# Kernel optimization log

Measured on AMD Instinct MI355X. Metric: run time of the kernel, lower is better.

The kernel has to match this reference:

```python
import jax, jax.numpy as jnp
import numpy as np

N = 50000
E = 800000
IN, HID, OUT = 256, 128, 64
BN_EPS = 1e-5

def sage(x, src, dst, Wl, bl, Wr):
    # PyG SAGEConv (aggr='mean'): lin_l(mean_j x_j) + lin_r(x_root)
    agg = jax.ops.segment_sum(x[src], dst, num_segments=N)
    deg = jax.ops.segment_sum(jnp.ones((src.shape[0], 1), x.dtype), dst, num_segments=N)
    mean_agg = agg / jnp.maximum(deg, 1.0)
    return mean_agg @ Wl + bl + x @ Wr

def bn_eval(x, gamma, beta):
    # eval-mode BatchNorm1d with running_mean=0, running_var=1
    return x * (gamma / jnp.sqrt(1.0 + BN_EPS)) + beta

def setup_inputs() -> dict:
    key = jax.random.key(0)
    ks = jax.random.split(key, 16)
    g = lambda k, shp, s: jax.random.normal(k, shp, jnp.float32) * s
    inp = {
        'x': g(ks[0], (N, IN), 1.0),
        'edge_index': jax.random.randint(ks[1], (2, E), 0, N, jnp.int32),
        'eps': g(ks[2], (10, N, OUT), 1.0),
        'W1l': g(ks[3], (IN, HID), 0.06), 'b1': jnp.zeros((HID,), jnp.float32), 'W1r': g(ks[4], (IN, HID), 0.06),
        'g1': jnp.ones((HID,), jnp.float32), 'be1': jnp.zeros((HID,), jnp.float32),
        'W2l': g(ks[5], (HID, 2 * HID), 0.09), 'b2': jnp.zeros((2 * HID,), jnp.float32), 'W2r': g(ks[6], (HID, 2 * HID), 0.09),
        'g2': jnp.ones((2 * HID,), jnp.float32), 'be2': jnp.zeros((2 * HID,), jnp.float32),
        'W3l': g(ks[7], (2 * HID, 2 * OUT), 0.06), 'b3': jnp.zeros((2 * OUT,), jnp.float32), 'W3r': g(ks[8], (2 * HID, 2 * OUT), 0.06),
        'Wd1': g(ks[9], (OUT, HID), 0.12), 'bd1': jnp.zeros((HID,), jnp.float32),
        'g3': jnp.ones((HID,), jnp.float32), 'be3': jnp.zeros((HID,), jnp.float32),
        'Wd2': g(ks[10], (HID, IN), 0.09), 'bd2': jnp.zeros((IN,), jnp.float32),
    }
    return inp

def reference(x, edge_index, eps, W1l, b1, W1r, g1, be1, W2l, b2, W2r, g2, be2,
              W3l, b3, W3r, Wd1, bd1, g3, be3, Wd2, bd2):
    src, dst = edge_index[0], edge_index[1]
    # encode (dropout is identity in eval mode)
    x1 = bn_eval(jax.nn.relu(sage(x, src, dst, W1l, b1, W1r)), g1, be1)
    x2 = bn_eval(jax.nn.relu(sage(x1, src, dst, W2l, b2, W2r)), g2, be2)
    mz = sage(x2, src, dst, W3l, b3, W3r)
    mean, log_std = mz[:, :OUT], mz[:, OUT:]
    # reparameterize: average of n_samples draws == mean + std * mean(eps)
    std = jnp.exp(log_std)
    z = mean + std * jnp.mean(eps, axis=0)
    # decode
    h = bn_eval(jax.nn.relu(z @ Wd1 + bd1), g3, be3) + x1
    return h @ Wd2 + bd2
```

## Files before the change

kernel.cpp:

```cpp
#include <hip/hip_runtime.h>


typedef unsigned short u16;
typedef short bf16x8 __attribute__((ext_vector_type(8)));
typedef float f32x4  __attribute__((ext_vector_type(4)));

constexpr float BN_EPS = 1e-5f;

__device__ __forceinline__ u16 f2bf(float f) {
    unsigned u = __float_as_uint(f);
    return (u16)((u + 0x7FFFu + ((u >> 16) & 1u)) >> 16);
}
__device__ __forceinline__ float bf2f(u16 h) {
    return __uint_as_float(((unsigned)h) << 16);
}
__device__ __forceinline__ void gl_lds16(const void* g, void* l) {
    __builtin_amdgcn_global_load_lds(
        (const __attribute__((address_space(1))) unsigned*)g,
        (__attribute__((address_space(3))) unsigned*)l, 16, 0, 0);
}

template<int KS>
__device__ __forceinline__ void stage_panel(const u16* g, char* lb, int k0, int t) {
    const int sr   = t >> 2;
    const int sq   = (t & 3) ^ ((t >> 3) & 3);
    const int wave = t >> 6;
    gl_lds16(g + (size_t)sr * KS + k0 + sq * 8,        lb + wave * 1024);
    gl_lds16(g + (size_t)(sr + 64) * KS + k0 + sq * 8, lb + 4096 + wave * 1024);
}


__global__ void hist_kernel(const int* __restrict__ dst, int E, int* __restrict__ deg) {
    int e = blockIdx.x * 256 + threadIdx.x;
    if (e < E) atomicAdd(&deg[dst[e]], 1);
}

__global__ __launch_bounds__(256)
void scan_partial(const int* __restrict__ deg, int N, int* __restrict__ bsum) {
    __shared__ int sd[256];
    int i = blockIdx.x * 256 + threadIdx.x;
    int v = (i < N) ? deg[i] : 0;
    sd[threadIdx.x] = v;
    __syncthreads();
    for (int off = 128; off > 0; off >>= 1) {
        if (threadIdx.x < off) sd[threadIdx.x] += sd[threadIdx.x + off];
        __syncthreads();
    }
    if (threadIdx.x == 0) bsum[blockIdx.x] = sd[0];
}

__global__ __launch_bounds__(256)
void scan_final2(const int* __restrict__ deg, const int* __restrict__ bsum,
                 int N, int E, int* __restrict__ row_ptr, int* __restrict__ cursor,
                 float* __restrict__ inv_deg) {
    __shared__ int sd[256];
    int t = threadIdx.x;
    int partial = 0;
    for (int j = t; j < blockIdx.x; j += 256) partial += bsum[j];
    sd[t] = partial;
    __syncthreads();
    for (int off = 128; off > 0; off >>= 1) {
        if (t < off) sd[t] += sd[t + off];
        __syncthreads();
    }
    int base = sd[0];
    __syncthreads();
    int i = blockIdx.x * 256 + t;
    int d = (i < N) ? deg[i] : 0;
    sd[t] = d;
    __syncthreads();
    for (int off = 1; off < 256; off <<= 1) {
        int u = (t >= off) ? sd[t - off] : 0;
        __syncthreads();
        sd[t] += u;
        __syncthreads();
    }
    if (i < N) {
        int excl = base + sd[t] - d;
        row_ptr[i] = excl;
        cursor[i]  = excl;
        inv_deg[i] = 1.0f / (float)max(d, 1);
        if (i == N - 1) row_ptr[N] = E;
    }
}

__global__ void fill_kernel(const int* __restrict__ src, const int* __restrict__ dst,
                            int E, int* __restrict__ cursor, int* __restrict__ csr) {
    int e = blockIdx.x * 256 + threadIdx.x;
    if (e < E) {
        int p = atomicAdd(&cursor[dst[e]], 1);
        csr[p] = src[e];
    }
}


__global__ void pack_cast(const float* __restrict__ x,
                          const float* __restrict__ W1l, const float* __restrict__ W1r,
                          const float* __restrict__ W2l, const float* __restrict__ W2r,
                          const float* __restrict__ W3l, const float* __restrict__ W3r,
                          const float* __restrict__ Wd1, const float* __restrict__ Wd2,
                          u16* __restrict__ Bt1, u16* __restrict__ Bt2,
                          u16* __restrict__ Bt3, u16* __restrict__ Btd1,
                          u16* __restrict__ Btd2, u16* __restrict__ xb,
                          int N, int Mpad) {
    int idx = blockIdx.x * 256 + threadIdx.x;
    if (idx < 65536) {
        int c = idx >> 8, k = idx & 255;
        float v = (c < 128) ? W1l[k * 128 + c] : W1r[k * 128 + (c - 128)];
        Bt1[c * 256 + k] = f2bf(v);
    } else if (idx < 131072) {
        int i2 = idx - 65536;
        int c = i2 >> 8, k = i2 & 255;
        float v = (k < 128) ? W2l[k * 256 + c] : W2r[(k - 128) * 256 + c];
        Bt2[c * 256 + k] = f2bf(v);
    } else if (idx < 196608) {
        int i2 = idx - 131072;
        int c = i2 >> 8, k = i2 & 255;
        float v = (c < 128) ? W3l[k * 128 + c] : W3r[k * 128 + (c - 128)];
        Bt3[c * 256 + k] = f2bf(v);
    } else if (idx < 204800) {
        int i2 = idx - 196608;
        int c = i2 >> 6, k = i2 & 63;
        Btd1[i2] = f2bf(Wd1[k * 128 + c]);
    } else if (idx < 237568) {
        int i2 = idx - 204800;
        int c = i2 >> 7, k = i2 & 127;
        Btd2[i2] = f2bf(Wd2[k * 256 + c]);
    }
    if (idx < Mpad * 64) {
        int row = idx >> 6, q = idx & 63;
        float4 v = make_float4(0.f, 0.f, 0.f, 0.f);
        if (row < N) v = *(const float4*)&x[(size_t)row * 256 + q * 4];
        ushort4 o;
        o.x = f2bf(v.x); o.y = f2bf(v.y); o.z = f2bf(v.z); o.w = f2bf(v.w);
        *(ushort4*)&xb[(size_t)row * 256 + q * 4] = o;
    }
}


template<int K, int NC, int EPI, bool F32OUT>
__global__ __launch_bounds__(256)
void mgemm(const u16* __restrict__ A, const u16* __restrict__ Bt,
           const float* __restrict__ bias, const float* __restrict__ gamma,
           const float* __restrict__ beta,
           const u16* __restrict__ skip, int skip_ld,
           void* __restrict__ Cout, int M) {
    __shared__ char lds[32768];
    char* As0 = lds;
    char* As1 = lds + 8192;
    char* Bs0 = lds + 16384;
    char* Bs1 = lds + 24576;

    const int t = threadIdx.x;
    const int l = t & 63;
    const int wave = t >> 6;
    const int wr = wave >> 1, wc = wave & 1;
    const int lr = l & 15, kg = l >> 4;
    const int row0 = blockIdx.x * 128;
    const int col0 = blockIdx.y * 128;

    f32x4 acc[4][4];
    #pragma unroll
    for (int m = 0; m < 4; m++)
        #pragma unroll
        for (int n = 0; n < 4; n++)
            #pragma unroll
            for (int r = 0; r < 4; r++) acc[m][n][r] = 0.f;

    const u16* Ab = A  + (size_t)row0 * K;
    const u16* Bb = Bt + (size_t)col0 * K;

    stage_panel<K>(Ab, As0, 0, t);
    stage_panel<K>(Bb, Bs0, 0, t);
    __syncthreads();

    const int swz = (kg ^ ((lr >> 1) & 3)) << 4;
    constexpr int NT = K / 32;
    for (int ks = 0; ks < NT; ks++) {
        char* Ac = (ks & 1) ? As1 : As0;
        char* Bc = (ks & 1) ? Bs1 : Bs0;
        if (ks + 1 < NT) {
            stage_panel<K>(Ab, (ks & 1) ? As0 : As1, (ks + 1) * 32, t);
            stage_panel<K>(Bb, (ks & 1) ? Bs0 : Bs1, (ks + 1) * 32, t);
        }
        bf16x8 af[4], bfr[4];
        #pragma unroll
        for (int m = 0; m < 4; m++)
            af[m] = *(const bf16x8*)(Ac + wr * 4096 + m * 1024 + lr * 64 + swz);
        #pragma unroll
        for (int n = 0; n < 4; n++)
            bfr[n] = *(const bf16x8*)(Bc + wc * 4096 + n * 1024 + lr * 64 + swz);
        #pragma unroll
        for (int m = 0; m < 4; m++)
            #pragma unroll
            for (int n = 0; n < 4; n++)
                acc[m][n] = __builtin_amdgcn_mfma_f32_16x16x32_bf16(
                    af[m], bfr[n], acc[m][n], 0, 0, 0);
        __syncthreads();
    }

    const float rs = rsqrtf(1.0f + BN_EPS);
    const int colb = col0 + wc * 64;
    const int rowb = row0 + wr * 64;
    float bia[4], gpr[4], bet[4];
    if (EPI == 1 || EPI == 2) {
        #pragma unroll
        for (int n = 0; n < 4; n++) {
            int c = colb + n * 16 + lr;
            bia[n] = bias[c];
            gpr[n] = gamma[c] * rs;
            bet[n] = beta[c];
        }
    } else if (EPI == 3) {
        #pragma unroll
        for (int n = 0; n < 4; n++) bia[n] = bias[colb + n * 16 + lr];
    }
    __syncthreads();

    char* rp = lds + wave * 4096;
    #pragma unroll
    for (int m = 0; m < 4; m++) {
        #pragma unroll
        for (int n = 0; n < 4; n++) {
            #pragma unroll
            for (int r = 0; r < 4; r++) {
                float v = acc[m][n][r];
                if (EPI == 1 || EPI == 2) {
                    v += bia[n];
                    v = fmaxf(v, 0.f);
                    v = v * gpr[n] + bet[n];
                }
                if (EPI == 2)
                    v += bf2f(skip[(size_t)(rowb + m * 16 + kg * 4 + r) * skip_ld
                                   + colb + n * 16 + lr]);
                if (EPI == 3) v += bia[n];
                int rl = kg * 4 + r, cl = n * 16 + lr;
                if (F32OUT) ((float*)rp)[rl * 64 + cl] = v;
                else        ((u16*)rp)[rl * 64 + cl]   = f2bf(v);
            }
        }
        if (F32OUT) {
            float* rpf = (float*)rp;
            #pragma unroll
            for (int rr = 0; rr < 4; rr++) {
                int rloc = rr * 4 + kg;
                int grow = rowb + m * 16 + rloc;
                if (grow < M) {
                    f32x4 v4 = *(f32x4*)&rpf[rloc * 64 + lr * 4];
                    *(f32x4*)((float*)Cout + (size_t)grow * NC + colb + lr * 4) = v4;
                }
            }
        } else {
            u16* rph = (u16*)rp;
            #pragma unroll
            for (int hh = 0; hh < 2; hh++) {
                int rloc = hh * 8 + (l >> 3);
                int grow = rowb + m * 16 + rloc;
                bf16x8 v8 = *(bf16x8*)&rph[rloc * 64 + (l & 7) * 8];
                *(bf16x8*)((u16*)Cout + (size_t)grow * NC + colb + (l & 7) * 8) = v8;
            }
        }
    }
}


__global__ __launch_bounds__(256)
void dec_fused(const u16* __restrict__ zb, const u16* __restrict__ Btd1,
               const u16* __restrict__ Btd2, const float* __restrict__ bd1,
               const float* __restrict__ g3, const float* __restrict__ be3,
               const u16* __restrict__ x1, const float* __restrict__ bd2,
               float* __restrict__ out, int M) {
    __shared__ char lds[65536];
    const int t = threadIdx.x;
    const int l = t & 63;
    const int wave = t >> 6;
    const int wr = wave >> 1, wc = wave & 1;
    const int lr = l & 15, kg = l >> 4;
    const int row0 = blockIdx.x * 128;
    const float rs = rsqrtf(1.0f + BN_EPS);
    const int swz = (kg ^ ((lr >> 1) & 3)) << 4;
    char* hb = lds + 32768;

    stage_panel<64>(zb + (size_t)row0 * 64, lds,         0, t);
    stage_panel<64>(zb + (size_t)row0 * 64, lds + 8192, 32, t);
    stage_panel<64>(Btd1, lds + 16384,  0, t);
    stage_panel<64>(Btd1, lds + 24576, 32, t);
    __syncthreads();

    f32x4 acc[4][4];
    #pragma unroll
    for (int m = 0; m < 4; m++)
        #pragma unroll
        for (int n = 0; n < 4; n++)
            #pragma unroll
            for (int r = 0; r < 4; r++) acc[m][n][r] = 0.f;

    #pragma unroll
    for (int ks = 0; ks < 2; ks++) {
        char* Ac = lds + ks * 8192;
        char* Bc = lds + 16384 + ks * 8192;
        bf16x8 af[4], bfr[4];
        #pragma unroll
        for (int m = 0; m < 4; m++)
            af[m] = *(const bf16x8*)(Ac + wr * 4096 + m * 1024 + lr * 64 + swz);
        #pragma unroll
        for (int n = 0; n < 4; n++)
            bfr[n] = *(const bf16x8*)(Bc + wc * 4096 + n * 1024 + lr * 64 + swz);
        #pragma unroll
        for (int m = 0; m < 4; m++)
            #pragma unroll
            for (int n = 0; n < 4; n++)
                acc[m][n] = __builtin_amdgcn_mfma_f32_16x16x32_bf16(
                    af[m], bfr[n], acc[m][n], 0, 0, 0);
    }

    {
        float bia[4], gpr[4], bet[4];
        #pragma unroll
        for (int n = 0; n < 4; n++) {
            int c = wc * 64 + n * 16 + lr;
            bia[n] = bd1[c];
            gpr[n] = g3[c] * rs;
            bet[n] = be3[c];
        }
        #pragma unroll
        for (int m = 0; m < 4; m++)
            #pragma unroll
            for (int n = 0; n < 4; n++)
                #pragma unroll
                for (int r = 0; r < 4; r++) {
                    int rl = wr * 64 + m * 16 + kg * 4 + r;
                    int cl = wc * 64 + n * 16 + lr;
                    float v = acc[m][n][r] + bia[n];
                    v = fmaxf(v, 0.f) * gpr[n] + bet[n];
                    v += bf2f(x1[(size_t)(row0 + rl) * 256 + cl]);
                    int slot = (cl >> 3) ^ (rl & 7);
                    ((u16*)(hb + rl * 256 + slot * 16))[cl & 7] = f2bf(v);
                }
    }
    __syncthreads();

    for (int ch = 0; ch < 2; ch++) {
        const u16* Bb2 = Btd2 + ch * 16384;
        stage_panel<128>(Bb2, lds, 0, t);
        #pragma unroll
        for (int m = 0; m < 4; m++)
            #pragma unroll
            for (int n = 0; n < 4; n++)
                #pragma unroll
                for (int r = 0; r < 4; r++) acc[m][n][r] = 0.f;
        __syncthreads();

        for (int ks = 0; ks < 4; ks++) {
            char* Bc = lds + (ks & 1) * 8192;
            if (ks + 1 < 4)
                stage_panel<128>(Bb2, lds + (((ks & 1) ^ 1) * 8192), (ks + 1) * 32, t);
            bf16x8 af[4], bfr[4];
            #pragma unroll
            for (int m = 0; m < 4; m++) {
                int row = wr * 64 + m * 16 + lr;
                int s = (ks * 4 + kg) ^ (row & 7);
                af[m] = *(const bf16x8*)(hb + row * 256 + s * 16);
            }
            #pragma unroll
            for (int n = 0; n < 4; n++)
                bfr[n] = *(const bf16x8*)(Bc + wc * 4096 + n * 1024 + lr * 64 + swz);
            #pragma unroll
            for (int m = 0; m < 4; m++)
                #pragma unroll
                for (int n = 0; n < 4; n++)
                    acc[m][n] = __builtin_amdgcn_mfma_f32_16x16x32_bf16(
                        af[m], bfr[n], acc[m][n], 0, 0, 0);
            __syncthreads();
        }

        const int colb = ch * 128 + wc * 64;
        const int rowb = row0 + wr * 64;
        float b2v[4];
        #pragma unroll
        for (int n = 0; n < 4; n++) b2v[n] = bd2[colb + n * 16 + lr];
        char* rp = lds + wave * 4096;
        #pragma unroll
        for (int m = 0; m < 4; m++) {
            #pragma unroll
            for (int n = 0; n < 4; n++)
                #pragma unroll
                for (int r = 0; r < 4; r++)
                    ((float*)rp)[(kg * 4 + r) * 64 + n * 16 + lr] = acc[m][n][r] + b2v[n];
            float* rpf = (float*)rp;
            #pragma unroll
            for (int rr = 0; rr < 4; rr++) {
                int rloc = rr * 4 + kg;
                int grow = rowb + m * 16 + rloc;
                if (grow < M) {
                    f32x4 v4 = *(f32x4*)&rpf[rloc * 64 + lr * 4];
                    *(f32x4*)&out[(size_t)grow * 256 + colb + lr * 4] = v4;
                }
            }
        }
        __syncthreads();
    }
}


__global__ __launch_bounds__(256)
void agg1_kernel(const u16* __restrict__ Y1, const int* __restrict__ row_ptr,
                 const int* __restrict__ csr, const float* __restrict__ inv_deg,
                 const float* __restrict__ b1, const float* __restrict__ g1,
                 const float* __restrict__ be1, u16* __restrict__ catX, int N) {
    int g   = (blockIdx.x * 256 + threadIdx.x) >> 4;
    int sub = threadIdx.x & 15;
    if (g >= N) return;
    int b = row_ptr[g], e = row_ptr[g + 1];
    const int off = sub * 8;
    float a[8] = {};
    int ee = b;
    for (; ee + 3 < e; ee += 4) {
        int j0 = csr[ee], j1 = csr[ee + 1], j2 = csr[ee + 2], j3 = csr[ee + 3];
        bf16x8 v0 = *(const bf16x8*)&Y1[(size_t)j0 * 256 + off];
        bf16x8 v1 = *(const bf16x8*)&Y1[(size_t)j1 * 256 + off];
        bf16x8 v2 = *(const bf16x8*)&Y1[(size_t)j2 * 256 + off];
        bf16x8 v3 = *(const bf16x8*)&Y1[(size_t)j3 * 256 + off];
        #pragma unroll
        for (int r = 0; r < 8; r++)
            a[r] += (bf2f((u16)v0[r]) + bf2f((u16)v1[r]))
                  + (bf2f((u16)v2[r]) + bf2f((u16)v3[r]));
    }
    for (; ee < e; ee++) {
        bf16x8 v0 = *(const bf16x8*)&Y1[(size_t)csr[ee] * 256 + off];
        #pragma unroll
        for (int r = 0; r < 8; r++) a[r] += bf2f((u16)v0[r]);
    }
    float id = inv_deg[g];
    bf16x8 u = *(const bf16x8*)&Y1[(size_t)g * 256 + 128 + off];
    const float rs = rsqrtf(1.0f + BN_EPS);
    bf16x8 o;
    #pragma unroll
    for (int r = 0; r < 8; r++) {
        int c = off + r;
        float v = a[r] * id + b1[c] + bf2f((u16)u[r]);
        v = fmaxf(v, 0.f);
        v = v * (g1[c] * rs) + be1[c];
        o[r] = (short)f2bf(v);
    }
    *(bf16x8*)&catX[(size_t)g * 256 + 128 + off] = o;
}

__global__ __launch_bounds__(256)
void agg2_kernel(const int* __restrict__ row_ptr, const int* __restrict__ csr,
                 const float* __restrict__ inv_deg, u16* __restrict__ catX, int N) {
    int g   = (blockIdx.x * 256 + threadIdx.x) >> 4;
    int sub = threadIdx.x & 15;
    if (g >= N) return;
    int b = row_ptr[g], e = row_ptr[g + 1];
    const int off = sub * 8;
    float a[8] = {};
    int ee = b;
    for (; ee + 3 < e; ee += 4) {
        int j0 = csr[ee], j1 = csr[ee + 1], j2 = csr[ee + 2], j3 = csr[ee + 3];
        bf16x8 v0 = *(const bf16x8*)&catX[(size_t)j0 * 256 + 128 + off];
        bf16x8 v1 = *(const bf16x8*)&catX[(size_t)j1 * 256 + 128 + off];
        bf16x8 v2 = *(const bf16x8*)&catX[(size_t)j2 * 256 + 128 + off];
        bf16x8 v3 = *(const bf16x8*)&catX[(size_t)j3 * 256 + 128 + off];
        #pragma unroll
        for (int r = 0; r < 8; r++)
            a[r] += (bf2f((u16)v0[r]) + bf2f((u16)v1[r]))
                  + (bf2f((u16)v2[r]) + bf2f((u16)v3[r]));
    }
    for (; ee < e; ee++) {
        bf16x8 v0 = *(const bf16x8*)&catX[(size_t)csr[ee] * 256 + 128 + off];
        #pragma unroll
        for (int r = 0; r < 8; r++) a[r] += bf2f((u16)v0[r]);
    }
    float id = inv_deg[g];
    bf16x8 o;
    #pragma unroll
    for (int r = 0; r < 8; r++) o[r] = (short)f2bf(a[r] * id);
    *(bf16x8*)&catX[(size_t)g * 256 + off] = o;
}

__global__ __launch_bounds__(256)
void agg3_kernel(const u16* __restrict__ Y3, const int* __restrict__ row_ptr,
                 const int* __restrict__ csr, const float* __restrict__ inv_deg,
                 const float* __restrict__ b3, const float* __restrict__ eps,
                 u16* __restrict__ z, int N) {
    int g   = (blockIdx.x * 256 + threadIdx.x) >> 4;
    int sub = threadIdx.x & 15;
    if (g >= N) return;
    int b = row_ptr[g], e = row_ptr[g + 1];
    const int off = sub * 8;

    f32x4 emv = {0.f, 0.f, 0.f, 0.f};
    #pragma unroll
    for (int t10 = 0; t10 < 10; t10++) {
        f32x4 v = *(const f32x4*)&eps[((size_t)t10 * N + g) * 64 + sub * 4];
        emv += v;
    }
    emv *= 0.1f;

    float a[8] = {};
    int ee = b;
    for (; ee + 3 < e; ee += 4) {
        int j0 = csr[ee], j1 = csr[ee + 1], j2 = csr[ee + 2], j3 = csr[ee + 3];
        bf16x8 v0 = *(const bf16x8*)&Y3[(size_t)j0 * 256 + off];
        bf16x8 v1 = *(const bf16x8*)&Y3[(size_t)j1 * 256 + off];
        bf16x8 v2 = *(const bf16x8*)&Y3[(size_t)j2 * 256 + off];
        bf16x8 v3 = *(const bf16x8*)&Y3[(size_t)j3 * 256 + off];
        #pragma unroll
        for (int r = 0; r < 8; r++)
            a[r] += (bf2f((u16)v0[r]) + bf2f((u16)v1[r]))
                  + (bf2f((u16)v2[r]) + bf2f((u16)v3[r]));
    }
    for (; ee < e; ee++) {
        bf16x8 v0 = *(const bf16x8*)&Y3[(size_t)csr[ee] * 256 + off];
        #pragma unroll
        for (int r = 0; r < 8; r++) a[r] += bf2f((u16)v0[r]);
    }
    float id = inv_deg[g];
    bf16x8 u = *(const bf16x8*)&Y3[(size_t)g * 256 + 128 + off];
    float mzv[8];
    #pragma unroll
    for (int r = 0; r < 8; r++)
        mzv[r] = a[r] * id + b3[off + r] + bf2f((u16)u[r]);

    const int wl = threadIdx.x & 63;
    const int wb = wl & ~15;
    const int s0 = wb + ((2 * sub) & 15);
    const int s1 = wb + ((2 * sub + 1) & 15);
    float em8[8];
    #pragma unroll
    for (int q = 0; q < 4; q++) {
        em8[q]     = __shfl(emv[q], s0);
        em8[4 + q] = __shfl(emv[q], s1);
    }
    float hi[8];
    #pragma unroll
    for (int r = 0; r < 8; r++) hi[r] = __shfl_xor(mzv[r], 8);

    if (sub < 8) {
        bf16x8 o;
        #pragma unroll
        for (int r = 0; r < 8; r++)
            o[r] = (short)f2bf(mzv[r] + expf(hi[r]) * em8[r]);
        *(bf16x8*)&z[(size_t)g * 64 + sub * 8] = o;
    }
}


extern "C" void kernel_launch(void* const* d_in, const int* in_sizes, int n_in,
                              void* d_out, int out_size, void* d_ws, size_t ws_size,
                              hipStream_t stream) {
    const float* x    = (const float*)d_in[0];
    const int*   ei   = (const int*)d_in[1];
    const float* eps  = (const float*)d_in[2];
    const float* W1l  = (const float*)d_in[3];
    const float* b1   = (const float*)d_in[4];
    const float* W1r  = (const float*)d_in[5];
    const float* g1   = (const float*)d_in[6];
    const float* be1  = (const float*)d_in[7];
    const float* W2l  = (const float*)d_in[8];
    const float* b2   = (const float*)d_in[9];
    const float* W2r  = (const float*)d_in[10];
    const float* g2   = (const float*)d_in[11];
    const float* be2  = (const float*)d_in[12];
    const float* W3l  = (const float*)d_in[13];
    const float* b3   = (const float*)d_in[14];
    const float* W3r  = (const float*)d_in[15];
    const float* Wd1  = (const float*)d_in[16];
    const float* bd1  = (const float*)d_in[17];
    const float* g3   = (const float*)d_in[18];
    const float* be3  = (const float*)d_in[19];
    const float* Wd2  = (const float*)d_in[20];
    const float* bd2  = (const float*)d_in[21];

    const int Nn   = in_sizes[0] / 256;
    const int E    = in_sizes[1] / 2;
    const int Mpad = ((Nn + 127) / 128) * 128;
    const int* srcp = ei;
    const int* dstp = ei + E;
    const int nb = (Nn + 255) / 256;

    char* w = (char*)d_ws;
    auto alloc = [&](size_t bytes) -> void* {
        void* p = (void*)w;
        w += (bytes + 255) & ~(size_t)255;
        return p;
    };
    int*   deg     = (int*)  alloc((size_t)Nn * 4);
    int*   bsum    = (int*)  alloc((size_t)nb * 4);
    int*   row_ptr = (int*)  alloc((size_t)(Nn + 1) * 4);
    int*   cursor  = (int*)  alloc((size_t)Nn * 4);
    float* inv_deg = (float*)alloc((size_t)Nn * 4);
    int*   csr     = (int*)  alloc((size_t)E * 4);
    u16*   Bt1     = (u16*)  alloc(256 * 256 * 2);
    u16*   Bt2     = (u16*)  alloc(256 * 256 * 2);
    u16*   Bt3     = (u16*)  alloc(256 * 256 * 2);
    u16*   Btd1    = (u16*)  alloc(128 * 64 * 2);
    u16*   Btd2    = (u16*)  alloc(256 * 128 * 2);
    u16*   xb      = (u16*)  alloc((size_t)Mpad * 256 * 2);
    u16*   zb      = (u16*)  alloc((size_t)Mpad * 64 * 2);
    u16*   bufA    = (u16*)  alloc((size_t)Mpad * 256 * 2);
    u16*   bufB    = (u16*)  alloc((size_t)Mpad * 256 * 2);
    u16*   bufC    = (u16*)  alloc((size_t)Mpad * 256 * 2);
    if ((size_t)(w - (char*)d_ws) > ws_size) return;

    hipMemsetAsync(deg, 0, (size_t)Nn * 4, stream);
    hist_kernel<<<(E + 255) / 256, 256, 0, stream>>>(dstp, E, deg);
    scan_partial<<<nb, 256, 0, stream>>>(deg, Nn, bsum);
    scan_final2<<<nb, 256, 0, stream>>>(deg, bsum, Nn, E, row_ptr, cursor, inv_deg);
    fill_kernel<<<(E + 255) / 256, 256, 0, stream>>>(srcp, dstp, E, cursor, csr);

    pack_cast<<<(Mpad * 64 + 255) / 256, 256, 0, stream>>>(
        x, W1l, W1r, W2l, W2r, W3l, W3r, Wd1, Wd2,
        Bt1, Bt2, Bt3, Btd1, Btd2, xb, Nn, Mpad);

    dim3 g2c(Mpad / 128, 2);
    const int aggBlocks = (Nn + 15) / 16;

    mgemm<256, 256, 0, false><<<g2c, 256, 0, stream>>>(
        xb, Bt1, nullptr, nullptr, nullptr, nullptr, 0, bufA, Mpad);
    agg1_kernel<<<aggBlocks, 256, 0, stream>>>(bufA, row_ptr, csr, inv_deg,
                                               b1, g1, be1, bufB, Nn);
    agg2_kernel<<<aggBlocks, 256, 0, stream>>>(row_ptr, csr, inv_deg, bufB, Nn);
    mgemm<256, 256, 1, false><<<g2c, 256, 0, stream>>>(
        bufB, Bt2, b2, g2, be2, nullptr, 0, bufA, Mpad);
    mgemm<256, 256, 0, false><<<g2c, 256, 0, stream>>>(
        bufA, Bt3, nullptr, nullptr, nullptr, nullptr, 0, bufC, Mpad);
    agg3_kernel<<<aggBlocks, 256, 0, stream>>>(bufC, row_ptr, csr, inv_deg,
                                               b3, eps, zb, Nn);
    dec_fused<<<Mpad / 128, 256, 0, stream>>>(
        zb, Btd1, Btd2, bd1, g3, be3, bufB + 128, bd2, (float*)d_out, Nn);
}
```

Measured before the change: 302.7 us.

## Fuse histogram into pack, degree-sort aggregation rows, fuse layer2/3 GEMMs

Merges the edge histogram into the weight/feature pack kernel to save a launch. Adds a degree-bucketed permutation so the aggregation kernels process nodes grouped by similar degree, which reduces divergence and load imbalance within a block. Fuses the layer-2 and layer-3 GEMMs into one kernel that keeps the intermediate activation in LDS, avoiding a global round trip. The fused GEMM uses 72KB of LDS, which may lower occupancy, and the permutation scatters output writes.

```diff
diff --git a/kernel.cpp b/kernel.cpp
--- a/kernel.cpp
+++ b/kernel.cpp
@@ -30,80 +30,18 @@
 }
 
 
-__global__ void hist_kernel(const int* __restrict__ dst, int E, int* __restrict__ deg) {
-    int e = blockIdx.x * 256 + threadIdx.x;
-    if (e < E) atomicAdd(&deg[dst[e]], 1);
-}
-
-__global__ __launch_bounds__(256)
-void scan_partial(const int* __restrict__ deg, int N, int* __restrict__ bsum) {
-    __shared__ int sd[256];
-    int i = blockIdx.x * 256 + threadIdx.x;
-    int v = (i < N) ? deg[i] : 0;
-    sd[threadIdx.x] = v;
-    __syncthreads();
-    for (int off = 128; off > 0; off >>= 1) {
-        if (threadIdx.x < off) sd[threadIdx.x] += sd[threadIdx.x + off];
-        __syncthreads();
-    }
-    if (threadIdx.x == 0) bsum[blockIdx.x] = sd[0];
-}
-
-__global__ __launch_bounds__(256)
-void scan_final2(const int* __restrict__ deg, const int* __restrict__ bsum,
-                 int N, int E, int* __restrict__ row_ptr, int* __restrict__ cursor,
-                 float* __restrict__ inv_deg) {
-    __shared__ int sd[256];
-    int t = threadIdx.x;
-    int partial = 0;
-    for (int j = t; j < blockIdx.x; j += 256) partial += bsum[j];
-    sd[t] = partial;
-    __syncthreads();
-    for (int off = 128; off > 0; off >>= 1) {
-        if (t < off) sd[t] += sd[t + off];
-        __syncthreads();
-    }
-    int base = sd[0];
-    __syncthreads();
-    int i = blockIdx.x * 256 + t;
-    int d = (i < N) ? deg[i] : 0;
-    sd[t] = d;
-    __syncthreads();
-    for (int off = 1; off < 256; off <<= 1) {
-        int u = (t >= off) ? sd[t - off] : 0;
-        __syncthreads();
-        sd[t] += u;
-        __syncthreads();
-    }
-    if (i < N) {
-        int excl = base + sd[t] - d;
-        row_ptr[i] = excl;
-        cursor[i]  = excl;
-        inv_deg[i] = 1.0f / (float)max(d, 1);
-        if (i == N - 1) row_ptr[N] = E;
-    }
-}
-
-__global__ void fill_kernel(const int* __restrict__ src, const int* __restrict__ dst,
-                            int E, int* __restrict__ cursor, int* __restrict__ csr) {
-    int e = blockIdx.x * 256 + threadIdx.x;
-    if (e < E) {
-        int p = atomicAdd(&cursor[dst[e]], 1);
-        csr[p] = src[e];
-    }
-}
-
-
-__global__ void pack_cast(const float* __restrict__ x,
-                          const float* __restrict__ W1l, const float* __restrict__ W1r,
-                          const float* __restrict__ W2l, const float* __restrict__ W2r,
-                          const float* __restrict__ W3l, const float* __restrict__ W3r,
-                          const float* __restrict__ Wd1, const float* __restrict__ Wd2,
-                          u16* __restrict__ Bt1, u16* __restrict__ Bt2,
-                          u16* __restrict__ Bt3, u16* __restrict__ Btd1,
-                          u16* __restrict__ Btd2, u16* __restrict__ xb,
-                          int N, int Mpad) {
+__global__ void histpack(const int* __restrict__ dst, int E, int* __restrict__ deg,
+                         const float* __restrict__ x,
+                         const float* __restrict__ W1l, const float* __restrict__ W1r,
+                         const float* __restrict__ W2l, const float* __restrict__ W2r,
+                         const float* __restrict__ W3l, const float* __restrict__ W3r,
+                         const float* __restrict__ Wd1, const float* __restrict__ Wd2,
+                         u16* __restrict__ Bt1, u16* __restrict__ Bt2,
+                         u16* __restrict__ Bt3, u16* __restrict__ Btd1,
+                         u16* __restrict__ Btd2, u16* __restrict__ xb,
+                         int N, int Mpad) {
     int idx = blockIdx.x * 256 + threadIdx.x;
+    if (idx < E) atomicAdd(&deg[dst[idx]], 1);
     if (idx < 65536) {
         int c = idx >> 8, k = idx & 255;
         float v = (c < 128) ? W1l[k * 128 + c] : W1r[k * 128 + (c - 128)];
@@ -137,13 +75,94 @@
     }
 }
 
-
-template<int K, int NC, int EPI, bool F32OUT>
+__global__ __launch_bounds__(256)
+void scan_partial(const int* __restrict__ deg, int N, int* __restrict__ bsum,
+                  int* __restrict__ bins) {
+    __shared__ int sd[256];
+    __shared__ int lbins[64];
+    int i = blockIdx.x * 256 + threadIdx.x;
+    int v = (i < N) ? deg[i] : 0;
+    sd[threadIdx.x] = v;
+    if (threadIdx.x < 64) lbins[threadIdx.x] = 0;
+    __syncthreads();
+    if (i < N) atomicAdd(&lbins[min(v, 63)], 1);
+    for (int off = 128; off > 0; off >>= 1) {
+        if (threadIdx.x < off) sd[threadIdx.x] += sd[threadIdx.x + off];
+        __syncthreads();
+    }
+    if (threadIdx.x == 0) bsum[blockIdx.x] = sd[0];
+    if (threadIdx.x < 64) {
+        int c = lbins[threadIdx.x];
+        if (c) atomicAdd(&bins[threadIdx.x], c);
+    }
+}
+
+__global__ void bin_scan(const int* __restrict__ bins, int* __restrict__ bincur) {
+    __shared__ int sd[64];
+    int t = threadIdx.x;
+    int v = bins[t];
+    sd[t] = v;
+    __syncthreads();
+    for (int off = 1; off < 64; off <<= 1) {
+        int u = (t >= off) ? sd[t - off] : 0;
+        __syncthreads();
+        sd[t] += u;
+        __syncthreads();
+    }
+    bincur[t] = sd[t] - v;
+}
+
+__global__ __launch_bounds__(256)
+void scan_final2(const int* __restrict__ deg, const int* __restrict__ bsum,
+                 int N, int E, int* __restrict__ row_ptr, int* __restrict__ cursor,
+                 float* __restrict__ inv_deg, int* __restrict__ bincur,
+                 int* __restrict__ perm) {
+    __shared__ int sd[256];
+    int t = threadIdx.x;
+    int partial = 0;
+    for (int j = t; j < blockIdx.x; j += 256) partial += bsum[j];
+    sd[t] = partial;
+    __syncthreads();
+    for (int off = 128; off > 0; off >>= 1) {
+        if (t < off) sd[t] += sd[t + off];
+        __syncthreads();
+    }
+    int base = sd[0];
+    __syncthreads();
+    int i = blockIdx.x * 256 + t;
+    int d = (i < N) ? deg[i] : 0;
+    sd[t] = d;
+    __syncthreads();
+    for (int off = 1; off < 256; off <<= 1) {
+        int u = (t >= off) ? sd[t - off] : 0;
+        __syncthreads();
+        sd[t] += u;
+        __syncthreads();
+    }
+    if (i < N) {
+        int excl = base + sd[t] - d;
+        row_ptr[i] = excl;
+        cursor[i]  = excl;
+        inv_deg[i] = 1.0f / (float)max(d, 1);
+        if (i == N - 1) row_ptr[N] = E;
+        int pos = atomicAdd(&bincur[min(d, 63)], 1);
+        perm[pos] = i;
+    }
+}
+
+__global__ void fill_kernel(const int* __restrict__ src, const int* __restrict__ dst,
+                            int E, int* __restrict__ cursor, int* __restrict__ csr) {
+    int e = blockIdx.x * 256 + threadIdx.x;
+    if (e < E) {
+        int p = atomicAdd(&cursor[dst[e]], 1);
+        csr[p] = src[e];
+    }
+}
+
+
+template<int K, int NC>
 __global__ __launch_bounds__(256)
 void mgemm(const u16* __restrict__ A, const u16* __restrict__ Bt,
-           const float* __restrict__ bias, const float* __restrict__ gamma,
-           const float* __restrict__ beta,
-           const u16* __restrict__ skip, int skip_ld,
            void* __restrict__ Cout, int M) {
     __shared__ char lds[32768];
     char* As0 = lds;
@@ -199,66 +218,176 @@
         __syncthreads();
     }
 
-    const float rs = rsqrtf(1.0f + BN_EPS);
     const int colb = col0 + wc * 64;
     const int rowb = row0 + wr * 64;
-    float bia[4], gpr[4], bet[4];
-    if (EPI == 1 || EPI == 2) {
+    __syncthreads();
+
+    char* rp = lds + wave * 4096;
+    #pragma unroll
+    for (int m = 0; m < 4; m++) {
+        #pragma unroll
+        for (int n = 0; n < 4; n++)
+            #pragma unroll
+            for (int r = 0; r < 4; r++) {
+                int rl = kg * 4 + r, cl = n * 16 + lr;
+                ((u16*)rp)[rl * 64 + cl] = f2bf(acc[m][n][r]);
+            }
+        u16* rph = (u16*)rp;
+        #pragma unroll
+        for (int hh = 0; hh < 2; hh++) {
+            int rloc = hh * 8 + (l >> 3);
+            int grow = rowb + m * 16 + rloc;
+            bf16x8 v8 = *(bf16x8*)&rph[rloc * 64 + (l & 7) * 8];
+            if (grow < M)
+                *(bf16x8*)((u16*)Cout + (size_t)grow * NC + colb + (l & 7) * 8) = v8;
+        }
+    }
+}
+
+
+__global__ __launch_bounds__(256)
+void gemm23(const u16* __restrict__ catX, const u16* __restrict__ Bt2,
+            const u16* __restrict__ Bt3,
+            const float* __restrict__ b2, const float* __restrict__ g2,
+            const float* __restrict__ be2,
+            u16* __restrict__ Y3, int M) {
+    __shared__ char lds[73728];
+    char* Ad0 = lds;
+    char* Ad1 = lds + 4096;
+    char* Bd0 = lds + 8192;
+    char* Bd1 = lds + 8192 + 16384;
+    char* hb  = lds + 40960;
+
+    const int t = threadIdx.x;
+    const int l = t & 63;
+    const int wave = t >> 6;
+    const int lr = l & 15, kg = l >> 4;
+    const int row0 = blockIdx.x * 64;
+    const int swz = (kg ^ ((lr >> 1) & 3)) << 4;
+    const int sr = t >> 2;
+    const int sq = (t & 3) ^ ((t >> 3) & 3);
+    const float rs = rsqrtf(1.0f + BN_EPS);
+
+    const u16* Ab = catX + (size_t)row0 * 256;
+
+    auto stageA = [&](char* buf, int k0) {
+        gl_lds16(Ab + (size_t)sr * 256 + k0 + sq * 8, buf + wave * 1024);
+    };
+    auto stageB = [&](const u16* Bt, char* buf, int k0) {
+        #pragma unroll
+        for (int q = 0; q < 4; q++)
+            gl_lds16(Bt + (size_t)(q * 64 + sr) * 256 + k0 + sq * 8,
+                     buf + q * 4096 + wave * 1024);
+    };
+
+    f32x4 acc[4][4];
+    #pragma unroll
+    for (int m = 0; m < 4; m++)
+        #pragma unroll
+        for (int n = 0; n < 4; n++)
+            #pragma unroll
+            for (int r = 0; r < 4; r++) acc[m][n][r] = 0.f;
+
+    stageA(Ad0, 0);
+    stageB(Bt2, Bd0, 0);
+    __syncthreads();
+    for (int ks = 0; ks < 8; ks++) {
+        char* Ac = (ks & 1) ? Ad1 : Ad0;
+        char* Bc = (ks & 1) ? Bd1 : Bd0;
+        if (ks < 7) {
+            stageA((ks & 1) ? Ad0 : Ad1, (ks + 1) * 32);
+            stageB(Bt2, (ks & 1) ? Bd0 : Bd1, (ks + 1) * 32);
+        }
+        bf16x8 af[4], bfr[4];
+        #pragma unroll
+        for (int m = 0; m < 4; m++)
+            af[m] = *(const bf16x8*)(Ac + m * 1024 + lr * 64 + swz);
+        #pragma unroll
+        for (int n = 0; n < 4; n++)
+            bfr[n] = *(const bf16x8*)(Bc + wave * 4096 + n * 1024 + lr * 64 + swz);
+        #pragma unroll
+        for (int m = 0; m < 4; m++)
+            #pragma unroll
+            for (int n = 0; n < 4; n++)
+                acc[m][n] = __builtin_amdgcn_mfma_f32_16x16x32_bf16(
+                    af[m], bfr[n], acc[m][n], 0, 0, 0);
+        __syncthreads();
+    }
+
+    stageB(Bt3, Bd0, 0);
+
+    {
+        float bia[4], gpr[4], bet[4];
         #pragma unroll
         for (int n = 0; n < 4; n++) {
-            int c = colb + n * 16 + lr;
-            bia[n] = bias[c];
-            gpr[n] = gamma[c] * rs;
-            bet[n] = beta[c];
-        }
-    } else if (EPI == 3) {
-        #pragma unroll
-        for (int n = 0; n < 4; n++) bia[n] = bias[colb + n * 16 + lr];
-    }
-    __syncthreads();
+            int c = wave * 64 + n * 16 + lr;
+            bia[n] = b2[c];
+            gpr[n] = g2[c] * rs;
+            bet[n] = be2[c];
+        }
+        #pragma unroll
+        for (int m = 0; m < 4; m++)
+            #pragma unroll
+            for (int n = 0; n < 4; n++)
+                #pragma unroll
+                for (int r = 0; r < 4; r++) {
+                    int rl = m * 16 + kg * 4 + r;
+                    int cl = wave * 64 + n * 16 + lr;
+                    float v = acc[m][n][r] + bia[n];
+                    v = fmaxf(v, 0.f) * gpr[n] + bet[n];
+                    int slot = (cl >> 3) ^ (rl & 7);
+                    ((u16*)(hb + rl * 512 + slot * 16))[cl & 7] = f2bf(v);
+                }
+    }
+    __syncthreads();
+
+    #pragma unroll
+    for (int m = 0; m < 4; m++)
+        #pragma unroll
+        for (int n = 0; n < 4; n++)
+            #pragma unroll
+            for (int r = 0; r < 4; r++) acc[m][n][r] = 0.f;
+
+    for (int ks = 0; ks < 8; ks++) {
+        char* Bc = (ks & 1) ? Bd1 : Bd0;
+        if (ks < 7) stageB(Bt3, (ks & 1) ? Bd0 : Bd1, (ks + 1) * 32);
+        bf16x8 af[4], bfr[4];
+        #pragma unroll
+        for (int m = 0; m < 4; m++) {
+            int row = m * 16 + lr;
+            int s = (ks * 4 + kg) ^ (row & 7);
+            af[m] = *(const bf16x8*)(hb + row * 512 + s * 16);
+        }
+        #pragma unroll
+        for (int n = 0; n < 4; n++)
+            bfr[n] = *(const bf16x8*)(Bc + wave * 4096 + n * 1024 + lr * 64 + swz);
+        #pragma unroll
+        for (int m = 0; m < 4; m++)
+            #pragma unroll
+            for (int n = 0; n < 4; n++)
+                acc[m][n] = __builtin_amdgcn_mfma_f32_16x16x32_bf16(
+                    af[m], bfr[n], acc[m][n], 0, 0, 0);
+        __syncthreads();
+    }
 
     char* rp = lds + wave * 4096;
     #pragma unroll
     for (int m = 0; m < 4; m++) {
         #pragma unroll
-        for (int n = 0; n < 4; n++) {
+        for (int n = 0; n < 4; n++)
             #pragma unroll
             for (int r = 0; r < 4; r++) {
-                float v = acc[m][n][r];
-                if (EPI == 1 || EPI == 2) {
-                    v += bia[n];
-                    v = fmaxf(v, 0.f);
-                    v = v * gpr[n] + bet[n];
-                }
-                if (EPI == 2)
-                    v += bf2f(skip[(size_t)(rowb + m * 16 + kg * 4 + r) * skip_ld
-                                   + colb + n * 16 + lr]);
-                if (EPI == 3) v += bia[n];
                 int rl = kg * 4 + r, cl = n * 16 + lr;
-                if (F32OUT) ((float*)rp)[rl * 64 + cl] = v;
-                else        ((u16*)rp)[rl * 64 + cl]   = f2bf(v);
+                ((u16*)rp)[rl * 64 + cl] = f2bf(acc[m][n][r]);
             }
-        }
-        if (F32OUT) {
-            float* rpf = (float*)rp;
-            #pragma unroll
-            for (int rr = 0; rr < 4; rr++) {
-                int rloc = rr * 4 + kg;
-                int grow = rowb + m * 16 + rloc;
-                if (grow < M) {
-                    f32x4 v4 = *(f32x4*)&rpf[rloc * 64 + lr * 4];
-                    *(f32x4*)((float*)Cout + (size_t)grow * NC + colb + lr * 4) = v4;
-                }
-            }
-        } else {
-            u16* rph = (u16*)rp;
-            #pragma unroll
-            for (int hh = 0; hh < 2; hh++) {
-                int rloc = hh * 8 + (l >> 3);
-                int grow = rowb + m * 16 + rloc;
-                bf16x8 v8 = *(bf16x8*)&rph[rloc * 64 + (l & 7) * 8];
-                *(bf16x8*)((u16*)Cout + (size_t)grow * NC + colb + (l & 7) * 8) = v8;
-            }
+        u16* rph = (u16*)rp;
+        #pragma unroll
+        for (int hh = 0; hh < 2; hh++) {
+            int rloc = hh * 8 + (l >> 3);
+            int grow = row0 + m * 16 + rloc;
+            bf16x8 v8 = *(bf16x8*)&rph[rloc * 64 + (l & 7) * 8];
+            if (grow < M)
+                *(bf16x8*)&Y3[(size_t)grow * 256 + wave * 64 + (l & 7) * 8] = v8;
         }
     }
 }
@@ -406,11 +535,13 @@
 __global__ __launch_bounds__(256)
 void agg1_kernel(const u16* __restrict__ Y1, const int* __restrict__ row_ptr,
                  const int* __restrict__ csr, const float* __restrict__ inv_deg,
+                 const int* __restrict__ perm,
                  const float* __restrict__ b1, const float* __restrict__ g1,
                  const float* __restrict__ be1, u16* __restrict__ catX, int N) {
-    int g   = (blockIdx.x * 256 + threadIdx.x) >> 4;
+    int gid = (blockIdx.x * 256 + threadIdx.x) >> 4;
     int sub = threadIdx.x & 15;
-    if (g >= N) return;
+    if (gid >= N) return;
+    int g = perm[gid];
     int b = row_ptr[g], e = row_ptr[g + 1];
     const int off = sub * 8;
     float a[8] = {};
@@ -448,10 +579,12 @@
 
 __global__ __launch_bounds__(256)
 void agg2_kernel(const int* __restrict__ row_ptr, const int* __restrict__ csr,
-                 const float* __restrict__ inv_deg, u16* __restrict__ catX, int N) {
-    int g   = (blockIdx.x * 256 + threadIdx.x) >> 4;
+                 const float* __restrict__ inv_deg, const int* __restrict__ perm,
+                 u16* __restrict__ catX, int N) {
+    int gid = (blockIdx.x * 256 + threadIdx.x) >> 4;
     int sub = threadIdx.x & 15;
-    if (g >= N) return;
+    if (gid >= N) return;
+    int g = perm[gid];
     int b = row_ptr[g], e = row_ptr[g + 1];
     const int off = sub * 8;
     float a[8] = {};
@@ -482,11 +615,13 @@
 __global__ __launch_bounds__(256)
 void agg3_kernel(const u16* __restrict__ Y3, const int* __restrict__ row_ptr,
                  const int* __restrict__ csr, const float* __restrict__ inv_deg,
+                 const int* __restrict__ perm,
                  const float* __restrict__ b3, const float* __restrict__ eps,
                  u16* __restrict__ z, int N) {
-    int g   = (blockIdx.x * 256 + threadIdx.x) >> 4;
+    int gid = (blockIdx.x * 256 + threadIdx.x) >> 4;
     int sub = threadIdx.x & 15;
-    if (g >= N) return;
+    if (gid >= N) return;
+    int g = perm[gid];
     int b = row_ptr[g], e = row_ptr[g + 1];
     const int off = sub * 8;
 
@@ -587,6 +722,9 @@
         return p;
     };
     int*   deg     = (int*)  alloc((size_t)Nn * 4);
+    int*   bins    = (int*)  alloc(64 * 4);
+    int*   bincur  = (int*)  alloc(64 * 4);
+    int*   perm    = (int*)  alloc((size_t)Nn * 4);
     int*   bsum    = (int*)  alloc((size_t)nb * 4);
     int*   row_ptr = (int*)  alloc((size_t)(Nn + 1) * 4);
     int*   cursor  = (int*)  alloc((size_t)Nn * 4);
@@ -604,29 +742,27 @@
     u16*   bufC    = (u16*)  alloc((size_t)Mpad * 256 * 2);
     if ((size_t)(w - (char*)d_ws) > ws_size) return;
 
-    hipMemsetAsync(deg, 0, (size_t)Nn * 4, stream);
-    hist_kernel<<<(E + 255) / 256, 256, 0, stream>>>(dstp, E, deg);
-    scan_partial<<<nb, 256, 0, stream>>>(deg, Nn, bsum);
-    scan_final2<<<nb, 256, 0, stream>>>(deg, bsum, Nn, E, row_ptr, cursor, inv_deg);
+    size_t degpad = ((size_t)Nn * 4 + 255) & ~(size_t)255;
+    hipMemsetAsync(deg, 0, degpad + 256, stream);
+
+    histpack<<<(Mpad * 64 + 255) / 256, 256, 0, stream>>>(
+        dstp, E, deg, x, W1l, W1r, W2l, W2r, W3l, W3r, Wd1, Wd2,
+        Bt1, Bt2, Bt3, Btd1, Btd2, xb, Nn, Mpad);
+    scan_partial<<<nb, 256, 0, stream>>>(deg, Nn, bsum, bins);
+    bin_scan<<<1, 64, 0, stream>>>(bins, bincur);
+    scan_final2<<<nb, 256, 0, stream>>>(deg, bsum, Nn, E, row_ptr, cursor,
+                                        inv_deg, bincur, perm);
     fill_kernel<<<(E + 255) / 256, 256, 0, stream>>>(srcp, dstp, E, cursor, csr);
-
-    pack_cast<<<(Mpad * 64 + 255) / 256, 256, 0, stream>>>(
-        x, W1l, W1r, W2l, W2r, W3l, W3r, Wd1, Wd2,
-        Bt1, Bt2, Bt3, Btd1, Btd2, xb, Nn, Mpad);
 
     dim3 g2c(Mpad / 128, 2);
     const int aggBlocks = (Nn + 15) / 16;
 
-    mgemm<256, 256, 0, false><<<g2c, 256, 0, stream>>>(
-        xb, Bt1, nullptr, nullptr, nullptr, nullptr, 0, bufA, Mpad);
-    agg1_kernel<<<aggBlocks, 256, 0, stream>>>(bufA, row_ptr, csr, inv_deg,
+    mgemm<256, 256><<<g2c, 256, 0, stream>>>(xb, Bt1, bufA, Mpad);
+    agg1_kernel<<<aggBlocks, 256, 0, stream>>>(bufA, row_ptr, csr, inv_deg, perm,
                                                b1, g1, be1, bufB, Nn);
-    agg2_kernel<<<aggBlocks, 256, 0, stream>>>(row_ptr, csr, inv_deg, bufB, Nn);
-    mgemm<256, 256, 1, false><<<g2c, 256, 0, stream>>>(
-        bufB, Bt2, b2, g2, be2, nullptr, 0, bufA, Mpad);
-    mgemm<256, 256, 0, false><<<g2c, 256, 0, stream>>>(
-        bufA, Bt3, nullptr, nullptr, nullptr, nullptr, 0, bufC, Mpad);
-    agg3_kernel<<<aggBlocks, 256, 0, stream>>>(bufC, row_ptr, csr, inv_deg,
+    agg2_kernel<<<aggBlocks, 256, 0, stream>>>(row_ptr, csr, inv_deg, perm, bufB, Nn);
+    gemm23<<<Mpad / 64, 256, 0, stream>>>(bufB, Bt2, Bt3, b2, g2, be2, bufC, Mpad);
+    agg3_kernel<<<aggBlocks, 256, 0, stream>>>(bufC, row_ptr, csr, inv_deg, perm,
                                                b3, eps, zb, Nn);
     dec_fused<<<Mpad / 128, 256, 0, stream>>>(
         zb, Btd1, Btd2, bd1, g3, be3, bufB + 128, bd2, (float*)d_out, Nn);
```

Result: slower. 420.9 us (+39.1%).
